# Kernel tuning notes

Hardware: AMD Instinct MI355X
Metric: run time of the kernel (lower is better)

The kernel has to match this reference:

```python
import jax, jax.numpy as jnp
import numpy as np

B, T, D = 4, 2048, 1024  # batch, seq_len, dec_dim_in == dim_proj_QK == dim_proj_V == dec_dim_out


def setup_inputs() -> dict:
    key = jax.random.key(0)
    ks = jax.random.split(key, 9)
    s = 1.0 / np.sqrt(D)  # torch Linear default init scale
    return {
        "x": jax.random.normal(ks[0], (B, T, D), dtype=jnp.float32),
        "Wq": jax.random.uniform(ks[1], (D, D), jnp.float32, -s, s),
        "bq": jax.random.uniform(ks[2], (D,), jnp.float32, -s, s),
        "Wk": jax.random.uniform(ks[3], (D, D), jnp.float32, -s, s),
        "bk": jax.random.uniform(ks[4], (D,), jnp.float32, -s, s),
        "Wv": jax.random.uniform(ks[5], (D, D), jnp.float32, -s, s),
        "bv": jax.random.uniform(ks[6], (D,), jnp.float32, -s, s),
        "Wh": jax.random.uniform(ks[7], (D, D), jnp.float32, -s, s),
        "bh": jax.random.uniform(ks[8], (D,), jnp.float32, -s, s),
    }


def reference(x, Wq, bq, Wk, bk, Wv, bv, Wh, bh):
    Q = x @ Wq + bq                      # [B, T, Dqk]
    K = x @ Wk + bk                      # [B, T, Dqk]
    V = x @ Wv + bv                      # [B, T, Dv]
    scale = 1.0 / jnp.sqrt(jnp.asarray(K.shape[-1], x.dtype))
    scores = jnp.einsum("btd,bsd->bts", Q, K) * scale  # [B, T, T]
    t = K.shape[1]
    causal = jnp.triu(jnp.ones((t, t), dtype=bool), k=1)  # True above diagonal
    scores = jnp.where(causal[None, :, :], -jnp.inf, scores)
    attn = jax.nn.softmax(scores, axis=-1)
    # dropout is identity in eval mode (reference baseline)
    out = jnp.einsum("bts,bsd->btd", attn, V)  # [B, T, Dv]
    return out @ Wh + bh
```

## Files before the change

### kernel.cpp

```cpp
#include <hip/hip_runtime.h>


typedef __attribute__((ext_vector_type(8)))  short short8;
typedef __attribute__((ext_vector_type(4)))  float f4;

#define BM 128
#define BN 128
#define BK 64
#define BM2 256
#define BN2 256

#define F_OBF    1
#define F_SKIP   2
#define F_KLIM   4
#define F_REVY   8
#define F_VSPL   16
#define F_RSCL   32
#define F_EXP    64
#define F_RSUM   128
#define F_SPLITK 256

#define WAITV8() asm volatile("s_waitcnt vmcnt(8)" ::: "memory")
#define WAITV0() asm volatile("s_waitcnt vmcnt(0)" ::: "memory")
#define BARR()   asm volatile("s_barrier" ::: "memory")

__device__ inline unsigned short f2bf(float f) {
    union { float f; unsigned u; } c; c.f = f;
    unsigned u = c.u;
    return (unsigned short)((u + 0x7fffu + ((u >> 16) & 1u)) >> 16);
}
__device__ inline float bf2f(unsigned short u) {
    union { unsigned u; float f; } c; c.u = ((unsigned)u) << 16;
    return c.f;
}
__device__ inline void gload16(const void* g, void* l) {
    __builtin_amdgcn_global_load_lds(
        (const __attribute__((address_space(1))) void*)g,
        (__attribute__((address_space(3))) void*)l,
        16, 0, 0);
}

template<int FLAGS>
__global__ __launch_bounds__(256)
void gemm_bt(const unsigned short* __restrict__ A,
             const unsigned short* __restrict__ Bt,
             void* __restrict__ C,
             const float* __restrict__ bias,
             int M, int N, int K, int lda, int ldb, int ldc,
             long sA, long sB, long sC,
             float scale,
             unsigned short* __restrict__ C2, long sC2, int Tv, int vsplit,
             float* __restrict__ rowsums)
{
    const int b = blockIdx.z;
    A  += (long)b * sA;
    Bt += (long)b * sB;
    if (FLAGS & (F_RSCL | F_RSUM)) rowsums += (long)b * M;

    int by = blockIdx.y;
    if (FLAGS & F_REVY) by = gridDim.y - 1 - by;
    const int m0 = by * BM;

    int n0, split = 0;
    if (FLAGS & F_SPLITK) {
        const int nbx = N / BN;
        n0 = (blockIdx.x % nbx) * BN;
        split = blockIdx.x / nbx;
        if (split && m0 < 1024) return;
    } else {
        n0 = blockIdx.x * BN;
    }

    if ((FLAGS & F_SKIP) && n0 > m0 + (BM - 1)) return;

    int kend = K;
    if (FLAGS & F_KLIM) { int ke = m0 + BM; kend = ke < K ? ke : K; }
    int kt0 = 0;
    if (FLAGS & F_SPLITK) {
        if (split == 0) { if (kend > 1024) kend = 1024; }
        else            { kt0 = 1024 / BK; }
    }
    const int kt1 = kend / BK;

    __shared__ unsigned short As[BM * BK];
    __shared__ unsigned short Bs[BN * BK];

    const int tid  = threadIdx.x;
    const int lane = tid & 63;
    const int wave = tid >> 6;
    const int wm   = wave & 1;
    const int wn   = wave >> 1;
    const int lrow = lane & 15;
    const int quad = lane >> 4;

    f4 acc[4][4];
#pragma unroll
    for (int i = 0; i < 4; ++i)
#pragma unroll
        for (int j = 0; j < 4; ++j) acc[i][j] = (f4)0.0f;

    const int srow = tid >> 3;
    const int gco  = ((tid & 7) ^ (srow & 7)) << 3;
    const int rdsl = (lrow & 7);

    for (int kt = kt0; kt < kt1; ++kt) {
        const int k0 = kt * BK;
#pragma unroll
        for (int d = 0; d < 4; ++d) {
            const int row = d * 32 + srow;
            const unsigned short* ga = A  + (long)(m0 + row) * lda + k0 + gco;
            const unsigned short* gb = Bt + (long)(n0 + row) * ldb + k0 + gco;
            const int ldsoff = (d * 256 + wave * 64) * 16;
            gload16(ga, (char*)As + ldsoff);
            gload16(gb, (char*)Bs + ldsoff);
        }
        __syncthreads();

#pragma unroll
        for (int ks = 0; ks < 2; ++ks) {
            const int slot = ((ks * 4 + quad) ^ rdsl) << 3;
            short8 af[4], bfr[4];
#pragma unroll
            for (int i = 0; i < 4; ++i) {
                af[i]  = *(const short8*)(As + (wm * 64 + i * 16 + lrow) * BK + slot);
                bfr[i] = *(const short8*)(Bs + (wn * 64 + i * 16 + lrow) * BK + slot);
            }
#pragma unroll
            for (int i = 0; i < 4; ++i)
#pragma unroll
                for (int j = 0; j < 4; ++j)
                    acc[i][j] = __builtin_amdgcn_mfma_f32_16x16x32_bf16(
                        af[i], bfr[j], acc[i][j], 0, 0, 0);
        }
        __syncthreads();
    }

    const int row0 = m0 + wm * 64 + quad * 4;
    const int col0 = n0 + wn * 64 + lrow;

    float bj[4];
#pragma unroll
    for (int j = 0; j < 4; ++j) bj[j] = bias ? bias[col0 + j * 16] : 0.0f;

    unsigned short* Cb = (unsigned short*)C;
    float*          Cf = (float*)C;
    const long cbase = (long)b * sC;

#pragma unroll
    for (int i = 0; i < 4; ++i) {
#pragma unroll
        for (int j = 0; j < 4; ++j) {
            const int col = col0 + j * 16;
#pragma unroll
            for (int r = 0; r < 4; ++r) {
                const int row = row0 + i * 16 + r;
                float v = acc[i][j][r] * scale + bj[j];
                const long off = cbase + (long)row * ldc + col;
                if (FLAGS & F_OBF) Cb[off] = f2bf(v);
                else               Cf[off] = v;
            }
        }
    }
}

template<int HA>
__device__ inline void lda_half(short8 (&af)[8], const unsigned short* Asb,
                                int wm, int lrow, int quad, int rdsl)
{
#pragma unroll
    for (int i = 0; i < 4; ++i)
#pragma unroll
        for (int ks = 0; ks < 2; ++ks)
            af[i * 2 + ks] = *(const short8*)(
                Asb + (wm * 128 + HA * 64 + i * 16 + lrow) * BK
                    + (((ks * 4 + quad) ^ rdsl) << 3));
}

template<int QB>
__device__ inline void ldb_q(short8 (&bq)[4], const unsigned short* Bsb,
                             int wn, int lrow, int quad, int rdsl)
{
#pragma unroll
    for (int j = 0; j < 2; ++j)
#pragma unroll
        for (int ks = 0; ks < 2; ++ks)
            bq[j * 2 + ks] = *(const short8*)(
                Bsb + (wn * 64 + QB * 32 + j * 16 + lrow) * BK
                    + (((ks * 4 + quad) ^ rdsl) << 3));
}

template<int HA, int QB>
__device__ inline void mfma16(f4 (&acc)[8][4], const short8 (&af)[8],
                              const short8 (&bq)[4])
{
#pragma unroll
    for (int i = 0; i < 4; ++i)
#pragma unroll
        for (int j = 0; j < 2; ++j)
#pragma unroll
            for (int ks = 0; ks < 2; ++ks)
                acc[HA * 4 + i][QB * 2 + j] =
                    __builtin_amdgcn_mfma_f32_16x16x32_bf16(
                        af[i * 2 + ks], bq[j * 2 + ks],
                        acc[HA * 4 + i][QB * 2 + j], 0, 0, 0);
}

__device__ inline void stage_tile256(const unsigned short* __restrict__ Arow,
                                     const unsigned short* __restrict__ Brow,
                                     int k0, unsigned short* As, unsigned short* Bs,
                                     int lda, int ldb, int tid)
{
    const int srow = tid >> 3;
    const int gco  = ((tid & 7) ^ (srow & 7)) << 3;
    const int wave = tid >> 6;
#pragma unroll
    for (int d = 0; d < 4; ++d) {
        const int row = d * 64 + srow;
        const int ldsoff = (d * 512 + wave * 64) * 16;
        gload16(Arow + (long)row * lda + k0 + gco, (char*)As + ldsoff);
        gload16(Brow + (long)row * ldb + k0 + gco, (char*)Bs + ldsoff);
    }
}

template<int FLAGS>
__global__ __launch_bounds__(512)
void gemm256(const unsigned short* __restrict__ A,
             const unsigned short* __restrict__ Bt,
             void* __restrict__ C,
             const float* __restrict__ bias,
             int M, int N, int K, int lda, int ldb, int ldc,
             long sA, long sB, long sC,
             float scale,
             unsigned short* __restrict__ C2, long sC2, int Tv, int vsplit,
             float* __restrict__ rowsums)
{
    const int b = blockIdx.z;
    A  += (long)b * sA;
    Bt += (long)b * sB;
    if (FLAGS & (F_RSCL | F_RSUM)) rowsums += (long)b * M;

    int by = blockIdx.y;
    if (FLAGS & F_REVY) by = gridDim.y - 1 - by;
    const int m0 = by * BM2;

    int n0, split = 0;
    if (FLAGS & F_SPLITK) {
        const int nbx = N / BN2;
        n0 = (blockIdx.x % nbx) * BN2;
        split = blockIdx.x / nbx;
        if (split && m0 < 1024) return;
    } else {
        n0 = blockIdx.x * BN2;
    }

    if ((FLAGS & F_SKIP) && n0 > m0 + (BM2 - 1)) return;

    int kend = K;
    if (FLAGS & F_KLIM) { int ke = m0 + BM2; kend = ke < K ? ke : K; }
    int kt0 = 0;
    if (FLAGS & F_SPLITK) {
        if (split == 0) { if (kend > 1024) kend = 1024; }
        else            { kt0 = 1024 / BK; }
    }
    const int kt1 = kend / BK;

    __shared__ unsigned short sm[4][BM2 * BK];

    const int tid  = threadIdx.x;
    const int lane = tid & 63;
    const int wave = tid >> 6;
    const int wm   = wave & 1;
    const int wn   = wave >> 1;
    const int lrow = lane & 15;
    const int quad = lane >> 4;
    const int rdsl = lrow & 7;

    f4 acc[8][4];
#pragma unroll
    for (int i = 0; i < 8; ++i)
#pragma unroll
        for (int j = 0; j < 4; ++j) acc[i][j] = (f4)0.0f;

    const unsigned short* Arow = A  + (long)m0 * lda;
    const unsigned short* Brow = Bt + (long)n0 * ldb;
    const int ktiles = kt1 - kt0;

    stage_tile256(Arow, Brow, kt0 * BK, sm[0], sm[1], lda, ldb, tid);
    if (ktiles > 1) {
        stage_tile256(Arow, Brow, (kt0 + 1) * BK, sm[2], sm[3], lda, ldb, tid);
        WAITV8();
    } else {
        WAITV0();
    }
    BARR();

    short8 af[8], bf0[4], bf1[4];
    for (int t = 0; t < ktiles; ++t) {
        const int cur = t & 1;
        const unsigned short* Asb = sm[cur * 2];
        const unsigned short* Bsb = sm[cur * 2 + 1];

        lda_half<0>(af, Asb, wm, lrow, quad, rdsl);
        ldb_q<0>(bf0, Bsb, wn, lrow, quad, rdsl);
        BARR();
        __builtin_amdgcn_s_setprio(1);
        mfma16<0, 0>(acc, af, bf0);
        __builtin_amdgcn_s_setprio(0);
        BARR();

        ldb_q<1>(bf1, Bsb, wn, lrow, quad, rdsl);
        BARR();
        __builtin_amdgcn_s_setprio(1);
        mfma16<0, 1>(acc, af, bf1);
        __builtin_amdgcn_s_setprio(0);
        BARR();

        lda_half<1>(af, Asb, wm, lrow, quad, rdsl);
        BARR();
        __builtin_amdgcn_s_setprio(1);
        mfma16<1, 1>(acc, af, bf1);
        __builtin_amdgcn_s_setprio(0);
        BARR();

        if (t + 2 < ktiles)
            stage_tile256(Arow, Brow, (kt0 + t + 2) * BK,
                          sm[cur * 2], sm[cur * 2 + 1], lda, ldb, tid);
        __builtin_amdgcn_s_setprio(1);
        mfma16<1, 0>(acc, af, bf0);
        __builtin_amdgcn_s_setprio(0);
        if (t + 2 < ktiles) WAITV8();
        else                WAITV0();
        BARR();
    }

    const int row0 = m0 + wm * 128 + quad * 4;
    const int col0 = n0 + wn * 64 + lrow;

    float bj[4];
#pragma unroll
    for (int j = 0; j < 4; ++j) bj[j] = bias ? bias[col0 + j * 16] : 0.0f;

    if ((FLAGS & F_VSPL) && n0 >= vsplit) {
        const int bidx  = m0 >> 11;
        const int tloc0 = (m0 & 2047) + wm * 128 + quad * 4;
#pragma unroll
        for (int j = 0; j < 4; ++j) {
            const int d = col0 + j * 16 - vsplit;
            unsigned short* base = C2 + (long)bidx * sC2 + (long)d * Tv;
#pragma unroll
            for (int i = 0; i < 8; ++i) {
                const int tt = tloc0 + i * 16;
                unsigned long long pk = 0;
#pragma unroll
                for (int r = 0; r < 4; ++r) {
                    float v = acc[i][j][r] * scale + bj[j];
                    pk |= (unsigned long long)f2bf(v) << (16 * r);
                }
                *(unsigned long long*)(base + tt) = pk;
            }
        }
        return;
    }

    float inv[32];
    if (FLAGS & F_RSCL) {
#pragma unroll
        for (int i = 0; i < 8; ++i)
#pragma unroll
            for (int r = 0; r < 4; ++r)
                inv[i * 4 + r] = rowsums[row0 + i * 16 + r];
    }

    float rs[32];
    if (FLAGS & F_RSUM) {
#pragma unroll
        for (int k = 0; k < 32; ++k) rs[k] = 0.0f;
    }

    unsigned short* Cb = (unsigned short*)C;
    float*          Cf = ((FLAGS & F_SPLITK) && split) ? (float*)C2 : (float*)C;
    const long cbase = (long)b * sC;

#pragma unroll
    for (int i = 0; i < 8; ++i) {
#pragma unroll
        for (int j = 0; j < 4; ++j) {
            const int col = col0 + j * 16;
#pragma unroll
            for (int r = 0; r < 4; ++r) {
                const int row = row0 + i * 16 + r;
                float v = acc[i][j][r] * scale;
                if (FLAGS & F_EXP) { v = __expf(v); if (col > row) v = 0.0f; }
                if (FLAGS & F_RSUM) rs[i * 4 + r] += v;
                if (FLAGS & F_RSCL) v *= inv[i * 4 + r];
                if (!((FLAGS & F_SPLITK) && split)) v += bj[j];
                const long off = cbase + (long)row * ldc + col;
                if (FLAGS & F_OBF) Cb[off] = f2bf(v);
                else               Cf[off] = v;
            }
        }
    }

    if (FLAGS & F_RSUM) {
#pragma unroll
        for (int k = 0; k < 32; ++k) {
            rs[k] += __shfl_xor(rs[k], 1);
            rs[k] += __shfl_xor(rs[k], 2);
            rs[k] += __shfl_xor(rs[k], 4);
            rs[k] += __shfl_xor(rs[k], 8);
        }
        if (lrow == 0) {
#pragma unroll
            for (int i = 0; i < 8; ++i)
#pragma unroll
                for (int r = 0; r < 4; ++r)
                    atomicAdd(&rowsums[row0 + i * 16 + r], rs[i * 4 + r]);
        }
    }
}

__global__ void combine_upper(float* __restrict__ out,
                              const float* __restrict__ part)
{
    const long base = ((long)blockIdx.y * 2048 + 1024) * 1024 / 4;
    const long i = base + blockIdx.x * 256 + threadIdx.x;
    f4 a = ((f4*)out)[i];
    f4 bb = ((const f4*)part)[i];
    a.x += bb.x; a.y += bb.y; a.z += bb.z; a.w += bb.w;
    ((f4*)out)[i] = a;
}

__global__ void recip_sums(float* __restrict__ s)
{
    const int i = blockIdx.x * 256 + threadIdx.x;
    s[i] = 1.0f / s[i];
}

__global__ void gemv_bhh(const unsigned short* __restrict__ Wht,
                         const float* __restrict__ bv,
                         const float* __restrict__ bh,
                         float* __restrict__ bhh)
{
    const int m = blockIdx.x;
    const int tid = threadIdx.x;
    const int lane = tid & 63, wave = tid >> 6;
    __shared__ float red[4];
    const unsigned short* row = Wht + (long)m * 1024;
    float s = 0.0f;
#pragma unroll
    for (int k = 0; k < 4; ++k) {
        const int idx = tid * 4 + k;
        s += bf2f(row[idx]) * bv[idx];
    }
    for (int o = 32; o > 0; o >>= 1) s += __shfl_down(s, o);
    if (lane == 0) red[wave] = s;
    __syncthreads();
    if (tid == 0) bhh[m] = red[0] + red[1] + red[2] + red[3] + bh[m];
}

__global__ void prep(const float* __restrict__ x,
                     const float* __restrict__ Wq, const float* __restrict__ Wk,
                     const float* __restrict__ Wv, const float* __restrict__ Wh,
                     const float* __restrict__ bq, const float* __restrict__ bk,
                     unsigned short* __restrict__ Xbf,
                     unsigned short* __restrict__ Wqkvt,
                     unsigned short* __restrict__ Wht,
                     unsigned short* __restrict__ Wvb,
                     float* __restrict__ bqkv)
{
    __shared__ unsigned short tsh[32][33];
    const int bid = blockIdx.x;
    const int tid = threadIdx.x;

    if (bid < 8192) {
        const int i = bid * 256 + tid;
        f4 v = ((const f4*)x)[i];
        unsigned long long p = (unsigned long long)f2bf(v.x)
                             | ((unsigned long long)f2bf(v.y) << 16)
                             | ((unsigned long long)f2bf(v.z) << 32)
                             | ((unsigned long long)f2bf(v.w) << 48);
        ((unsigned long long*)Xbf)[i] = p;
    } else if (bid < 9216) {
        const int i = (bid - 8192) * 256 + tid;
        f4 v = ((const f4*)Wv)[i];
        unsigned long long p = (unsigned long long)f2bf(v.x)
                             | ((unsigned long long)f2bf(v.y) << 16)
                             | ((unsigned long long)f2bf(v.z) << 32)
                             | ((unsigned long long)f2bf(v.w) << 48);
        ((unsigned long long*)Wvb)[i] = p;
    } else if (bid < 12288) {
        const int wi = bid - 9216;
        const int w = wi >> 10, tile = wi & 1023;
        const float* src = (w == 0) ? Wq : (w == 1) ? Wk : Wh;
        unsigned short* dst = (w == 0) ? Wqkvt : (w == 1) ? (Wqkvt + 1024 * 1024) : Wht;
        const int c0 = (tile & 31) * 32, r0 = (tile >> 5) * 32;
        const int xx = tid & 31, yy = tid >> 5;
        for (int i = yy; i < 32; i += 8)
            tsh[i][xx] = f2bf(src[(long)(r0 + i) * 1024 + c0 + xx]);
        __syncthreads();
        for (int i = yy; i < 32; i += 8)
            dst[(long)(c0 + i) * 1024 + r0 + xx] = tsh[xx][i];
    } else {
        const int i = (bid - 12288) * 256 + tid;
        if (i < 1024) { bqkv[i] = bq[i]; bqkv[1024 + i] = bk[i]; bqkv[2048 + i] = 0.0f; }
    }
}

extern "C" void kernel_launch(void* const* d_in, const int* in_sizes, int n_in,
                              void* d_out, int out_size, void* d_ws, size_t ws_size,
                              hipStream_t stream)
{
    const float* x  = (const float*)d_in[0];
    const float* Wq = (const float*)d_in[1];
    const float* bq = (const float*)d_in[2];
    const float* Wk = (const float*)d_in[3];
    const float* bk = (const float*)d_in[4];
    const float* Wv = (const float*)d_in[5];
    const float* bv = (const float*)d_in[6];
    const float* Wh = (const float*)d_in[7];
    const float* bh = (const float*)d_in[8];
    float* out = (float*)d_out;

    const int  Bb = 4, T = 2048, Dm = 1024;
    const long BT = (long)Bb * T;

    unsigned short* ws = (unsigned short*)d_ws;
    size_t o = 0;
    unsigned short* Xbf   = ws + o; o += (size_t)BT * Dm;
    unsigned short* Wqkvt = ws + o; o += (size_t)3 * Dm * Dm;
    unsigned short* Wht   = ws + o; o += (size_t)Dm * Dm;
    unsigned short* Wvb   = ws + o; o += (size_t)Dm * Dm;
    float* bqkv = (float*)(ws + o); o += (size_t)3 * Dm * 2;
    float* bhh  = (float*)(ws + o); o += (size_t)Dm * 2;
    float* sums = (float*)(ws + o); o += (size_t)BT * 2;
    unsigned short* QKV   = ws + o; o += (size_t)BT * 3 * Dm;
    unsigned short* Vt    = ws + o; o += (size_t)BT * Dm;
    unsigned short* Pp    = ws + o; o += (size_t)Bb * T * T;
    float* part = (float*)(ws + o);

    const dim3 blk(256);
    const dim3 blk2(512);
    const long sRow3 = (long)T * 3 * Dm;

    hipMemsetAsync(sums, 0, (size_t)BT * sizeof(float), stream);

    prep<<<12289, blk, 0, stream>>>(x, Wq, Wk, Wv, Wh, bq, bk,
                                    Xbf, Wqkvt, Wht, Wvb, bqkv);

    gemm_bt<F_OBF><<<dim3(Dm / BN, Dm / BM, 1), blk, 0, stream>>>(
        Wht, Wvb, Wqkvt + 2 * Dm * Dm, nullptr, Dm, Dm, Dm, Dm, Dm, Dm,
        0, 0, 0, 1.0f, nullptr, 0, 0, 0, nullptr);

    gemv_bhh<<<Dm, blk, 0, stream>>>(Wht, bv, bh, bhh);

    gemm256<F_OBF | F_VSPL><<<dim3(3 * Dm / BN2, BT / BM2, 1), blk2, 0, stream>>>(
        Xbf, Wqkvt, QKV, bqkv, (int)BT, 3 * Dm, Dm, Dm, Dm, 3 * Dm,
        0, 0, 0, 1.0f, Vt, (long)Dm * T, T, 2 * Dm, nullptr);

    gemm256<F_OBF | F_SKIP | F_REVY | F_EXP | F_RSUM>
        <<<dim3(T / BN2, T / BM2, Bb), blk2, 0, stream>>>(
        QKV, QKV + Dm, Pp, nullptr, T, T, Dm, 3 * Dm, 3 * Dm, T,
        sRow3, sRow3, (long)T * T, 1.0f / 32.0f,
        nullptr, 0, 0, 0, sums);

    recip_sums<<<dim3((int)(BT / 256)), blk, 0, stream>>>(sums);

    gemm256<F_KLIM | F_REVY | F_RSCL | F_SPLITK>
        <<<dim3(2 * Dm / BN2, T / BM2, Bb), blk2, 0, stream>>>(
        Pp, Vt, out, bhh, T, Dm, T, T, T, Dm,
        (long)T * T, (long)Dm * T, (long)T * Dm, 1.0f,
        (unsigned short*)part, 0, 0, 0, sums);

    combine_upper<<<dim3(1024, Bb), blk, 0, stream>>>(out, part);
}
```

Before: 299.5 us.

## Unroll gemm256 main loop by two with cross-tile fragment prefetch

```diff
diff --git a/kernel.cpp b/kernel.cpp
--- a/kernel.cpp
+++ b/kernel.cpp
@@ -22,7 +22,9 @@
 
 #define WAITV8() asm volatile("s_waitcnt vmcnt(8)" ::: "memory")
 #define WAITV0() asm volatile("s_waitcnt vmcnt(0)" ::: "memory")
-#define BARR()   asm volatile("s_barrier" ::: "memory")
+#define SBAR()   __builtin_amdgcn_s_barrier()
+#define PRIO1()  __builtin_amdgcn_s_setprio(1)
+#define PRIO0()  __builtin_amdgcn_s_setprio(0)
 
 __device__ inline unsigned short f2bf(float f) {
     union { float f; unsigned u; } c; c.f = f;
@@ -55,32 +57,13 @@
     const int b = blockIdx.z;
     A  += (long)b * sA;
     Bt += (long)b * sB;
-    if (FLAGS & (F_RSCL | F_RSUM)) rowsums += (long)b * M;
 
     int by = blockIdx.y;
     if (FLAGS & F_REVY) by = gridDim.y - 1 - by;
     const int m0 = by * BM;
-
-    int n0, split = 0;
-    if (FLAGS & F_SPLITK) {
-        const int nbx = N / BN;
-        n0 = (blockIdx.x % nbx) * BN;
-        split = blockIdx.x / nbx;
-        if (split && m0 < 1024) return;
-    } else {
-        n0 = blockIdx.x * BN;
-    }
-
-    if ((FLAGS & F_SKIP) && n0 > m0 + (BM - 1)) return;
-
-    int kend = K;
-    if (FLAGS & F_KLIM) { int ke = m0 + BM; kend = ke < K ? ke : K; }
-    int kt0 = 0;
-    if (FLAGS & F_SPLITK) {
-        if (split == 0) { if (kend > 1024) kend = 1024; }
-        else            { kt0 = 1024 / BK; }
-    }
-    const int kt1 = kend / BK;
+    const int n0 = blockIdx.x * BN;
+
+    const int kt1 = K / BK;
 
     __shared__ unsigned short As[BM * BK];
     __shared__ unsigned short Bs[BN * BK];
@@ -103,7 +86,7 @@
     const int gco  = ((tid & 7) ^ (srow & 7)) << 3;
     const int rdsl = (lrow & 7);
 
-    for (int kt = kt0; kt < kt1; ++kt) {
+    for (int kt = 0; kt < kt1; ++kt) {
         const int k0 = kt * BK;
 #pragma unroll
         for (int d = 0; d < 4; ++d) {
@@ -189,20 +172,18 @@
                     + (((ks * 4 + quad) ^ rdsl) << 3));
 }
 
-template<int HA, int QB>
-__device__ inline void mfma16(f4 (&acc)[8][4], const short8 (&af)[8],
-                              const short8 (&bq)[4])
-{
-#pragma unroll
-    for (int i = 0; i < 4; ++i)
-#pragma unroll
-        for (int j = 0; j < 2; ++j)
-#pragma unroll
-            for (int ks = 0; ks < 2; ++ks)
-                acc[HA * 4 + i][QB * 2 + j] =
-                    __builtin_amdgcn_mfma_f32_16x16x32_bf16(
-                        af[i * 2 + ks], bq[j * 2 + ks],
-                        acc[HA * 4 + i][QB * 2 + j], 0, 0, 0);
+template<int RI, int CJ>
+__device__ inline void mfma_cl(f4 (&acc)[8][4], const short8 (&a)[8],
+                               const short8 (&b)[4])
+{
+#pragma unroll
+    for (int ks = 0; ks < 2; ++ks)
+#pragma unroll
+        for (int i = 0; i < 4; ++i)
+#pragma unroll
+            for (int j = 0; j < 2; ++j)
+                acc[RI + i][CJ + j] = __builtin_amdgcn_mfma_f32_16x16x32_bf16(
+                    a[i * 2 + ks], b[j * 2 + ks], acc[RI + i][CJ + j], 0, 0, 0);
 }
 
 __device__ inline void stage_tile256(const unsigned short* __restrict__ Arow,
@@ -223,7 +204,7 @@
 }
 
 template<int FLAGS>
-__global__ __launch_bounds__(512)
+__global__ __launch_bounds__(512, 2)
 void gemm256(const unsigned short* __restrict__ A,
              const unsigned short* __restrict__ Bt,
              void* __restrict__ C,
@@ -285,52 +266,64 @@
     const unsigned short* Brow = Bt + (long)n0 * ldb;
     const int ktiles = kt1 - kt0;
 
+    short8 aLo[8], aHi[8], bA[4], bB[4];
+
     stage_tile256(Arow, Brow, kt0 * BK, sm[0], sm[1], lda, ldb, tid);
-    if (ktiles > 1) {
-        stage_tile256(Arow, Brow, (kt0 + 1) * BK, sm[2], sm[3], lda, ldb, tid);
-        WAITV8();
-    } else {
-        WAITV0();
-    }
-    BARR();
-
-    short8 af[8], bf0[4], bf1[4];
-    for (int t = 0; t < ktiles; ++t) {
-        const int cur = t & 1;
-        const unsigned short* Asb = sm[cur * 2];
-        const unsigned short* Bsb = sm[cur * 2 + 1];
-
-        lda_half<0>(af, Asb, wm, lrow, quad, rdsl);
-        ldb_q<0>(bf0, Bsb, wn, lrow, quad, rdsl);
-        BARR();
-        __builtin_amdgcn_s_setprio(1);
-        mfma16<0, 0>(acc, af, bf0);
-        __builtin_amdgcn_s_setprio(0);
-        BARR();
-
-        ldb_q<1>(bf1, Bsb, wn, lrow, quad, rdsl);
-        BARR();
-        __builtin_amdgcn_s_setprio(1);
-        mfma16<0, 1>(acc, af, bf1);
-        __builtin_amdgcn_s_setprio(0);
-        BARR();
-
-        lda_half<1>(af, Asb, wm, lrow, quad, rdsl);
-        BARR();
-        __builtin_amdgcn_s_setprio(1);
-        mfma16<1, 1>(acc, af, bf1);
-        __builtin_amdgcn_s_setprio(0);
-        BARR();
-
-        if (t + 2 < ktiles)
-            stage_tile256(Arow, Brow, (kt0 + t + 2) * BK,
-                          sm[cur * 2], sm[cur * 2 + 1], lda, ldb, tid);
-        __builtin_amdgcn_s_setprio(1);
-        mfma16<1, 0>(acc, af, bf0);
-        __builtin_amdgcn_s_setprio(0);
-        if (t + 2 < ktiles) WAITV8();
-        else                WAITV0();
-        BARR();
+    stage_tile256(Arow, Brow, (kt0 + 1) * BK, sm[2], sm[3], lda, ldb, tid);
+    WAITV8();
+    SBAR();
+    lda_half<0>(aLo, sm[0], wm, lrow, quad, rdsl);
+    ldb_q<0>(bA, sm[1], wn, lrow, quad, rdsl);
+
+    for (int it = 0; it < ktiles; it += 2) {
+        ldb_q<1>(bB, sm[1], wn, lrow, quad, rdsl);
+        SBAR();
+        PRIO1(); mfma_cl<0, 0>(acc, aLo, bA); PRIO0();
+        SBAR();
+        lda_half<1>(aHi, sm[0], wm, lrow, quad, rdsl);
+        SBAR();
+        PRIO1(); mfma_cl<0, 2>(acc, aLo, bB); PRIO0();
+        SBAR();
+        PRIO1(); mfma_cl<4, 2>(acc, aHi, bB); PRIO0();
+        SBAR();
+        if (it + 2 < ktiles) {
+            stage_tile256(Arow, Brow, (kt0 + it + 2) * BK, sm[0], sm[1],
+                          lda, ldb, tid);
+            WAITV8();
+        } else {
+            WAITV0();
+        }
+        SBAR();
+        lda_half<0>(aLo, sm[2], wm, lrow, quad, rdsl);
+        ldb_q<0>(bB, sm[3], wn, lrow, quad, rdsl);
+        PRIO1(); mfma_cl<4, 0>(acc, aHi, bA); PRIO0();
+        SBAR();
+
+        ldb_q<1>(bA, sm[3], wn, lrow, quad, rdsl);
+        SBAR();
+        PRIO1(); mfma_cl<0, 0>(acc, aLo, bB); PRIO0();
+        SBAR();
+        lda_half<1>(aHi, sm[2], wm, lrow, quad, rdsl);
+        SBAR();
+        PRIO1(); mfma_cl<0, 2>(acc, aLo, bA); PRIO0();
+        SBAR();
+        PRIO1(); mfma_cl<4, 2>(acc, aHi, bA); PRIO0();
+        SBAR();
+        const bool more = (it + 2 < ktiles);
+        if (it + 3 < ktiles) {
+            stage_tile256(Arow, Brow, (kt0 + it + 3) * BK, sm[2], sm[3],
+                          lda, ldb, tid);
+            WAITV8();
+        } else {
+            WAITV0();
+        }
+        SBAR();
+        if (more) {
+            lda_half<0>(aLo, sm[0], wm, lrow, quad, rdsl);
+            ldb_q<0>(bA, sm[1], wn, lrow, quad, rdsl);
+        }
+        PRIO1(); mfma_cl<4, 0>(acc, aHi, bB); PRIO0();
+        SBAR();
     }
 
     const int row0 = m0 + wm * 128 + quad * 4;
```

New measurement: 492.0 us. +64.2%, slower.
